# Kernel optimization log

Measured on AMD Instinct MI355X. Metric: run time of the kernel, lower is better.

## Reference

```python
import jax, jax.numpy as jnp
import numpy as np

C = 512  # channels

def _maxpool2x2(x):
    # x: [B,H,W,C] -> [B,H/2,W/2,C]
    B, H, W, Cc = x.shape
    return x.reshape(B, H // 2, 2, W // 2, 2, Cc).max(axis=(2, 4))

def setup_inputs() -> dict:
    key = jax.random.key(0)
    ks = jax.random.split(key, 6)
    x = jax.random.normal(ks[0], (16, 64, 64, C), dtype=jnp.float32)
    # 1x1 conv kernels stored as [C_in, C_out]; spectral norm treated as identity
    # on the (already-normalized) effective weights.
    s = lambda k, i, o: jax.random.normal(k, (i, o), dtype=jnp.float32) / np.sqrt(i)
    W_theta = s(ks[1], C, C // 8)
    W_phi = s(ks[2], C, C // 8)
    W_g = s(ks[3], C, C // 2)
    W_o = s(ks[4], C // 2, C)
    gamma = jnp.float32(0.7)  # nonzero so the attention path matters
    return {"x": x, "W_theta": W_theta, "W_phi": W_phi, "W_g": W_g,
            "W_o": W_o, "gamma": gamma}

def reference(x, W_theta, W_phi, W_g, W_o, gamma):
    B, H, W, Cc = x.shape
    S = H * W            # query length
    Sk = S // 4          # key/value length after 2x2 maxpool
    theta = jnp.einsum('bhwc,cd->bhwd', x, W_theta)              # [B,H,W,C/8]
    phi = _maxpool2x2(jnp.einsum('bhwc,cd->bhwd', x, W_phi))     # [B,H/2,W/2,C/8]
    g = _maxpool2x2(jnp.einsum('bhwc,cd->bhwd', x, W_g))         # [B,H/2,W/2,C/2]
    theta = theta.reshape(B, S, Cc // 8)
    phi = phi.reshape(B, Sk, Cc // 8)
    g = g.reshape(B, Sk, Cc // 2)
    # scores [B,S,Sk]; SAGAN omits the 1/sqrt(d_k) scaling
    beta = jax.nn.softmax(jnp.einsum('bqd,bkd->bqk', theta, phi), axis=-1)
    tmp = jnp.einsum('bqk,bkv->bqv', beta, g).reshape(B, H, W, Cc // 2)
    o = jnp.einsum('bhwv,vc->bhwc', tmp, W_o)
    return gamma * o + x
```

## Files before the change

kernel.cpp:

```cpp
#include <hip/hip_runtime.h>

typedef __attribute__((ext_vector_type(8))) short bf16x8;
typedef __attribute__((ext_vector_type(4))) float f32x4;
typedef unsigned short u16;
typedef unsigned int u32;

#define MFMA __builtin_amdgcn_mfma_f32_16x16x32_bf16

static __device__ __forceinline__ float b2f(u16 u) {
    u32 x = ((u32)u) << 16;
    return __builtin_bit_cast(float, x);
}
static __device__ __forceinline__ u16 f2b(float f) {
    u32 u = __builtin_bit_cast(u32, f);
    u32 r = (u + 0x7fffu + ((u >> 16) & 1u)) >> 16;
    return (u16)r;
}
static __device__ __forceinline__ void async16(const u16* g, u16* l) {
    __builtin_amdgcn_global_load_lds(
        (const __attribute__((address_space(1))) u32*)g,
        (__attribute__((address_space(3))) u32*)l, 16, 0, 0);
}

__global__ void pack_w(const float* __restrict__ Wt, const float* __restrict__ Wp,
                       const float* __restrict__ Wg, const float* __restrict__ Wo,
                       u16* __restrict__ WcatT, u16* __restrict__ WoT) {
    int t = blockIdx.x * 256 + threadIdx.x;
    const int n1 = 384 * 512;
    if (t < n1) {
        int n = t >> 9, k = t & 511;
        float v;
        if (n < 64)       v = Wt[k * 64 + n];
        else if (n < 128) v = Wp[k * 64 + (n - 64)];
        else              v = Wg[k * 256 + (n - 128)];
        WcatT[t] = f2b(v);
    } else {
        int j = t - n1;
        if (j < 512 * 256) {
            int n = j >> 8, k = j & 255;
            WoT[j] = f2b(Wo[k * 512 + n]);
        }
    }
}

template <int K>
static __device__ __forceinline__ void gemm_core(const u16* __restrict__ A,
                                                 const u16* __restrict__ Bt,
                                                 int m0, int n0, int lda, int ldb,
                                                 f32x4 acc[4][4], u16* S) {
    const int t = threadIdx.x;
    const int w = t >> 6, li = t & 15, quad = (t >> 4) & 3;
    const int wm = (w & 1) << 6, wn = (w >> 1) << 6;
#pragma unroll
    for (int mi = 0; mi < 4; mi++)
#pragma unroll
        for (int ni = 0; ni < 4; ni++) acc[mi][ni] = (f32x4)0.0f;
    const u16* ag = A + (size_t)(m0 + (t >> 2)) * lda + ((t & 3) << 3);
    const u16* bg = Bt + (size_t)(n0 + (t >> 2)) * ldb + ((t & 3) << 3);
    const int ws = w * 512;
    async16(ag, S + ws);
    async16(ag + (size_t)64 * lda, S + ws + 2048);
    async16(bg, S + 4096 + ws);
    async16(bg + (size_t)64 * ldb, S + 4096 + ws + 2048);
    __syncthreads();
    int cur = 0;
#pragma unroll
    for (int k0 = 0; k0 < K; k0 += 32) {
        if (k0 + 32 < K) {
            u16* nS = S + (cur ^ 1) * 8192;
            async16(ag + k0 + 32, nS + ws);
            async16(ag + k0 + 32 + (size_t)64 * lda, nS + ws + 2048);
            async16(bg + k0 + 32, nS + 4096 + ws);
            async16(bg + k0 + 32 + (size_t)64 * ldb, nS + 4096 + ws + 2048);
        }
        const u16* As = S + cur * 8192;
        const u16* Bs = As + 4096;
        bf16x8 af[4], bfr[4];
#pragma unroll
        for (int mi = 0; mi < 4; mi++)
            af[mi] = *(const bf16x8*)(As + (wm + mi * 16 + li) * 32 + quad * 8);
#pragma unroll
        for (int ni = 0; ni < 4; ni++)
            bfr[ni] = *(const bf16x8*)(Bs + (wn + ni * 16 + li) * 32 + quad * 8);
#pragma unroll
        for (int mi = 0; mi < 4; mi++)
#pragma unroll
            for (int ni = 0; ni < 4; ni++)
                acc[mi][ni] = MFMA(af[mi], bfr[ni], acc[mi][ni], 0, 0, 0);
        __syncthreads();
        cur ^= 1;
    }
}

template <int K>
static __device__ __forceinline__ void gemm_core_f32(const float* __restrict__ A,
                                                     const u16* __restrict__ Bt,
                                                     int m0, int n0, int lda, int ldb,
                                                     f32x4 acc[4][4], u16* S) {
    const int t = threadIdx.x;
    const int w = t >> 6, li = t & 15, quad = (t >> 4) & 3;
    const int wm = (w & 1) << 6, wn = (w >> 1) << 6;
#pragma unroll
    for (int mi = 0; mi < 4; mi++)
#pragma unroll
        for (int ni = 0; ni < 4; ni++) acc[mi][ni] = (f32x4)0.0f;
    const float* ag = A + (size_t)(m0 + (t >> 2)) * lda + ((t & 3) << 3);
    const u16* bg = Bt + (size_t)(n0 + (t >> 2)) * ldb + ((t & 3) << 3);
    const int ws = w * 512;
    {
        f32x4 a00 = *(const f32x4*)(ag);
        f32x4 a01 = *(const f32x4*)(ag + 4);
        f32x4 a10 = *(const f32x4*)(ag + (size_t)64 * lda);
        f32x4 a11 = *(const f32x4*)(ag + (size_t)64 * lda + 4);
        async16(bg, S + 4096 + ws);
        async16(bg + (size_t)64 * ldb, S + 4096 + ws + 2048);
        bf16x8 v0, v1;
#pragma unroll
        for (int e = 0; e < 4; e++) {
            v0[e] = (short)f2b(a00[e]); v0[4 + e] = (short)f2b(a01[e]);
            v1[e] = (short)f2b(a10[e]); v1[4 + e] = (short)f2b(a11[e]);
        }
        *(bf16x8*)(S + t * 8) = v0;
        *(bf16x8*)(S + 2048 + t * 8) = v1;
    }
    __syncthreads();
    int cur = 0;
#pragma unroll
    for (int k0 = 0; k0 < K; k0 += 32) {
        f32x4 a00, a01, a10, a11;
        if (k0 + 32 < K) {
            a00 = *(const f32x4*)(ag + k0 + 32);
            a01 = *(const f32x4*)(ag + k0 + 36);
            a10 = *(const f32x4*)(ag + k0 + 32 + (size_t)64 * lda);
            a11 = *(const f32x4*)(ag + k0 + 36 + (size_t)64 * lda);
            u16* nS = S + (cur ^ 1) * 8192;
            async16(bg + k0 + 32, nS + 4096 + ws);
            async16(bg + k0 + 32 + (size_t)64 * ldb, nS + 4096 + ws + 2048);
        }
        const u16* As = S + cur * 8192;
        const u16* Bs = As + 4096;
        bf16x8 af[4], bfr[4];
#pragma unroll
        for (int mi = 0; mi < 4; mi++)
            af[mi] = *(const bf16x8*)(As + (wm + mi * 16 + li) * 32 + quad * 8);
#pragma unroll
        for (int ni = 0; ni < 4; ni++)
            bfr[ni] = *(const bf16x8*)(Bs + (wn + ni * 16 + li) * 32 + quad * 8);
#pragma unroll
        for (int mi = 0; mi < 4; mi++)
#pragma unroll
            for (int ni = 0; ni < 4; ni++)
                acc[mi][ni] = MFMA(af[mi], bfr[ni], acc[mi][ni], 0, 0, 0);
        if (k0 + 32 < K) {
            u16* nS = S + (cur ^ 1) * 8192;
            bf16x8 v0, v1;
#pragma unroll
            for (int e = 0; e < 4; e++) {
                v0[e] = (short)f2b(a00[e]); v0[4 + e] = (short)f2b(a01[e]);
                v1[e] = (short)f2b(a10[e]); v1[4 + e] = (short)f2b(a11[e]);
            }
            *(bf16x8*)(nS + t * 8) = v0;
            *(bf16x8*)(nS + 2048 + t * 8) = v1;
        }
        __syncthreads();
        cur ^= 1;
    }
}

__global__ __launch_bounds__(256) void proj_gemm(const float* __restrict__ x,
                                                 const u16* __restrict__ WcatT,
                                                 u16* __restrict__ theta,
                                                 u16* __restrict__ phi,
                                                 u16* __restrict__ gT) {
    __shared__ __attribute__((aligned(16))) u16 S[16384];
    int bid = blockIdx.x;
    int sbid = (bid & 7) * 192 + (bid >> 3);
    int bm = sbid / 3, bn = sbid % 3;
    int m0 = bm * 128;
    f32x4 acc[4][4];
    gemm_core_f32<512>(x, WcatT, m0, bn * 128, 512, 512, acc, S);

    const int t = threadIdx.x;
    const int w = t >> 6, li = t & 15, quad = (t >> 4) & 3;
    const int cbase = (w >> 1) << 6;
    const int rbase = (w & 1) << 6;
#pragma unroll
    for (int mi = 0; mi < 4; mi++)
#pragma unroll
        for (int ni = 0; ni < 4; ni++) {
            int c = cbase + ni * 16 + li;
            int ch = c >> 3, ce = c & 7;
#pragma unroll
            for (int r = 0; r < 4; r++) {
                int lr = rbase + mi * 16 + quad * 4 + r;
                S[lr * 128 + ((ch ^ (lr & 7)) << 3) + ce] = f2b(acc[mi][ni][r]);
            }
        }
    __syncthreads();

    const int b = bm >> 5;
    if (bn == 0) {
        int lr = t >> 1;
#pragma unroll
        for (int k = 0; k < 4; k++) {
            int ch = (t & 1) * 4 + k;
            bf16x8 v = *(const bf16x8*)(S + lr * 128 + ((ch ^ (lr & 7)) << 3));
            *(bf16x8*)(theta + (size_t)(m0 + lr) * 64 + (t & 1) * 32 + k * 8) = v;
        }
        int w2 = t >> 3;
        int chp = 8 + (t & 7);
        int r0 = 2 * w2, r1 = r0 + 1, r2 = r0 + 64, r3 = r0 + 65;
        bf16x8 v0 = *(const bf16x8*)(S + r0 * 128 + ((chp ^ (r0 & 7)) << 3));
        bf16x8 v1 = *(const bf16x8*)(S + r1 * 128 + ((chp ^ (r1 & 7)) << 3));
        bf16x8 v2 = *(const bf16x8*)(S + r2 * 128 + ((chp ^ (r2 & 7)) << 3));
        bf16x8 v3 = *(const bf16x8*)(S + r3 * 128 + ((chp ^ (r3 & 7)) << 3));
        bf16x8 pv;
#pragma unroll
        for (int e = 0; e < 8; e++) {
            float mv = fmaxf(fmaxf(b2f((u16)v0[e]), b2f((u16)v1[e])),
                             fmaxf(b2f((u16)v2[e]), b2f((u16)v3[e])));
            pv[e] = (short)f2b(mv);
        }
        int pos2 = (bm & 31) * 32 + w2;
        *(bf16x8*)(phi + ((size_t)(b << 10) + pos2) * 64 + (t & 7) * 8) = pv;
    } else {
        const int c = t >> 1;
        const int poff = (t & 1) * 16;
        const int ch = c >> 3, ce = c & 7;
        u16 vals[16] __attribute__((aligned(16)));
#pragma unroll
        for (int j = 0; j < 16; j++) {
            int w2 = poff + j;
            int r0 = 2 * w2, r1 = r0 + 1, r2 = r0 + 64, r3 = r0 + 65;
            float m0v = b2f(S[r0 * 128 + ((ch ^ (r0 & 7)) << 3) + ce]);
            float m1v = b2f(S[r1 * 128 + ((ch ^ (r1 & 7)) << 3) + ce]);
            float m2v = b2f(S[r2 * 128 + ((ch ^ (r2 & 7)) << 3) + ce]);
            float m3v = b2f(S[r3 * 128 + ((ch ^ (r3 & 7)) << 3) + ce]);
            vals[j] = f2b(fmaxf(fmaxf(m0v, m1v), fmaxf(m2v, m3v)));
        }
        int cg = (bn - 1) * 128 + c;
        int pos2b = (bm & 31) * 32 + poff;
        u16* dst = gT + ((size_t)(b << 8) + cg) * 1024 + pos2b;
        *(uint4*)dst = *(const uint4*)vals;
        *(uint4*)(dst + 8) = *(const uint4*)(vals + 8);
    }
}

__global__ __launch_bounds__(256, 2) void attn_fused(const u16* __restrict__ theta,
                                                     const u16* __restrict__ phi,
                                                     const u16* __restrict__ gT,
                                                     u16* __restrict__ tmp) {
    __shared__ __attribute__((aligned(16))) u16 lds[28672];
    u16* stgP = lds;
    u16* stgG = lds + 4096;
    u16* pbuf = lds + 20480;

    int bid = blockIdx.x;
    int swz = (bid & 7) * 64 + (bid >> 3);
    int b = swz >> 5;
    int q0 = (swz & 31) << 7;
    const int t = threadIdx.x;
    const int w = t >> 6, li = t & 15, quad = (t >> 4) & 3;

    const u16* thp = theta + (((size_t)(b << 12) + q0 + w * 32 + li) << 6) + quad * 8;
    bf16x8 tq[2][2];
    tq[0][0] = *(const bf16x8*)thp;
    tq[0][1] = *(const bf16x8*)(thp + 32);
    tq[1][0] = *(const bf16x8*)(thp + (16 << 6));
    tq[1][1] = *(const bf16x8*)(thp + (16 << 6) + 32);

    const int srow = t >> 3;
    const int sc = (t & 7) ^ (srow & 7);
    const u16* phisrc = phi + ((size_t)(b << 10) + srow) * 64 + sc * 8;
    const u16* gsrc = gT + ((size_t)(b << 8) + srow) * 1024 + sc * 8;
    u16* pbq[2] = {pbuf + (w * 2 + 0) * 1024, pbuf + (w * 2 + 1) * 1024};

    f32x4 o[2][16];
#pragma unroll
    for (int qg = 0; qg < 2; qg++)
#pragma unroll
        for (int ni = 0; ni < 16; ni++) o[qg][ni] = (f32x4)0.0f;
    float m[2] = {-3.0e38f, -3.0e38f}, sum[2] = {0.0f, 0.0f};

    for (int kc = 0; kc < 16; kc++) {
        __syncthreads();
        async16(phisrc + (size_t)(kc * 64) * 64, stgP + w * 512);
        async16(phisrc + (size_t)(kc * 64 + 32) * 64, stgP + 2048 + w * 512);
#pragma unroll
        for (int j = 0; j < 8; j++)
            async16(gsrc + (size_t)(j * 32) * 1024 + kc * 64, stgG + j * 2048 + w * 512);
        __syncthreads();

        f32x4 sacc[2][4];
#pragma unroll
        for (int qg = 0; qg < 2; qg++)
#pragma unroll
            for (int nf = 0; nf < 4; nf++) sacc[qg][nf] = (f32x4)0.0f;
#pragma unroll
        for (int nf = 0; nf < 4; nf++) {
            int row = nf * 16 + li;
            int p0 = quad ^ (li & 7);
            int p1 = (4 + quad) ^ (li & 7);
            bf16x8 f0 = *(const bf16x8*)(stgP + row * 64 + p0 * 8);
            bf16x8 f1 = *(const bf16x8*)(stgP + row * 64 + p1 * 8);
            sacc[0][nf] = MFMA(f0, tq[0][0], sacc[0][nf], 0, 0, 0);
            sacc[0][nf] = MFMA(f1, tq[0][1], sacc[0][nf], 0, 0, 0);
            sacc[1][nf] = MFMA(f0, tq[1][0], sacc[1][nf], 0, 0, 0);
            sacc[1][nf] = MFMA(f1, tq[1][1], sacc[1][nf], 0, 0, 0);
        }

#pragma unroll
        for (int qg = 0; qg < 2; qg++) {
            float mc = sacc[qg][0][0];
#pragma unroll
            for (int nf = 0; nf < 4; nf++)
#pragma unroll
                for (int r = 0; r < 4; r++) mc = fmaxf(mc, sacc[qg][nf][r]);
            mc = fmaxf(mc, __shfl_xor(mc, 16, 64));
            mc = fmaxf(mc, __shfl_xor(mc, 32, 64));
            if (!__all(mc <= m[qg] + 8.0f)) {
                float nm = fmaxf(m[qg], mc);
                float f = __expf(m[qg] - nm);
                sum[qg] *= f;
#pragma unroll
                for (int ni = 0; ni < 16; ni++)
#pragma unroll
                    for (int r = 0; r < 4; r++) o[qg][ni][r] *= f;
                m[qg] = nm;
            }
            float p[16];
            float s = 0.0f;
#pragma unroll
            for (int nf = 0; nf < 4; nf++)
#pragma unroll
                for (int r = 0; r < 4; r++) {
                    float e = __expf(sacc[qg][nf][r] - m[qg]);
                    p[nf * 4 + r] = e;
                    s += e;
                }
            s += __shfl_xor(s, 16, 64);
            s += __shfl_xor(s, 32, 64);
            sum[qg] += s;

            u16* pb = pbq[qg];
#pragma unroll
            for (int nf = 0; nf < 4; nf++) {
                int cc = nf * 2 + (quad >> 1);
                int pos = cc ^ (li & 7);
                u32* dst = (u32*)(pb + li * 64 + pos * 8 + (quad & 1) * 4);
                dst[0] = (u32)f2b(p[nf * 4 + 0]) | ((u32)f2b(p[nf * 4 + 1]) << 16);
                dst[1] = (u32)f2b(p[nf * 4 + 2]) | ((u32)f2b(p[nf * 4 + 3]) << 16);
            }
        }

#pragma unroll
        for (int w2 = 0; w2 < 2; w2++) {
            int pos8 = ((w2 * 4 + quad) ^ (li & 7)) * 8;
            bf16x8 pf0 = *(const bf16x8*)(pbq[0] + li * 64 + pos8);
            bf16x8 pf1 = *(const bf16x8*)(pbq[1] + li * 64 + pos8);
#pragma unroll
            for (int ni = 0; ni < 16; ni++) {
                bf16x8 gf = *(const bf16x8*)(stgG + (ni * 16 + li) * 64 + pos8);
                o[0][ni] = MFMA(gf, pf0, o[0][ni], 0, 0, 0);
                o[1][ni] = MFMA(gf, pf1, o[1][ni], 0, 0, 0);
            }
        }
    }

    float inv[2] = {1.0f / sum[0], 1.0f / sum[1]};
#pragma unroll
    for (int qg = 0; qg < 2; qg++)
#pragma unroll
        for (int ni = 0; ni < 16; ni++)
#pragma unroll
            for (int r = 0; r < 4; r++) o[qg][ni][r] *= inv[qg];

    __syncthreads();
    u16* eb = lds + w * 4224;
    const int lane = t & 63;
#pragma unroll
    for (int qg = 0; qg < 2; qg++) {
#pragma unroll
        for (int ni = 0; ni < 16; ni++) {
            u32* d = (u32*)(eb + li * 264 + ni * 16 + quad * 4);
            d[0] = (u32)f2b(o[qg][ni][0]) | ((u32)f2b(o[qg][ni][1]) << 16);
            d[1] = (u32)f2b(o[qg][ni][2]) | ((u32)f2b(o[qg][ni][3]) << 16);
        }
#pragma unroll
        for (int pss = 0; pss < 8; pss++) {
            int row = pss * 2 + (lane >> 5);
            bf16x8 v = *(const bf16x8*)(eb + row * 264 + (lane & 31) * 8);
            *(bf16x8*)(tmp + ((size_t)(b << 12) + q0 + w * 32 + qg * 16 + row) * 256 +
                       (lane & 31) * 8) = v;
        }
    }
}

__global__ __launch_bounds__(256) void out_gemm(const u16* __restrict__ tmp,
                                                const u16* __restrict__ WoT,
                                                const float* __restrict__ x,
                                                const float* __restrict__ gamma_p,
                                                float* __restrict__ out) {
    __shared__ __attribute__((aligned(16))) u16 sbuf[16384];
    int bid = blockIdx.x;
    int sbid = (bid & 7) * 256 + (bid >> 3);
    int bm = sbid >> 2, bn = sbid & 3;
    f32x4 acc[4][4];
    gemm_core<256>(tmp, WoT, bm * 128, bn * 128, 256, 256, acc, sbuf);
    float gamma = gamma_p[0];
    const int t = threadIdx.x;
    const int w = t >> 6, li = t & 15, quad = (t >> 4) & 3;
    int row0 = bm * 128 + (w & 1) * 64;
    int col0 = bn * 128 + (w >> 1) * 64;
    float* fb = (float*)sbuf + w * 1088;
    const int lane = t & 63;
    const int rhi = lane >> 4, cl = (lane & 15) * 4;
#pragma unroll
    for (int mi = 0; mi < 4; mi++) {
        f32x4 xv[4];
#pragma unroll
        for (int j = 0; j < 4; j++) {
            size_t go = (size_t)(row0 + mi * 16 + j * 4 + rhi) * 512 + col0 + cl;
            xv[j] = *(const f32x4*)(x + go);
        }
#pragma unroll
        for (int ni = 0; ni < 4; ni++)
#pragma unroll
            for (int r = 0; r < 4; r++)
                fb[(quad * 4 + r) * 68 + ni * 16 + li] = acc[mi][ni][r];
#pragma unroll
        for (int j = 0; j < 4; j++) {
            f32x4 v = *(const f32x4*)(fb + (j * 4 + rhi) * 68 + cl);
#pragma unroll
            for (int e = 0; e < 4; e++) v[e] = gamma * v[e] + xv[j][e];
            size_t go = (size_t)(row0 + mi * 16 + j * 4 + rhi) * 512 + col0 + cl;
            *(f32x4*)(out + go) = v;
        }
    }
}

extern "C" void kernel_launch(void* const* d_in, const int* in_sizes, int n_in,
                              void* d_out, int out_size, void* d_ws, size_t ws_size,
                              hipStream_t stream) {
    (void)in_sizes; (void)n_in; (void)out_size; (void)ws_size;
    const float* x  = (const float*)d_in[0];
    const float* Wt = (const float*)d_in[1];
    const float* Wp = (const float*)d_in[2];
    const float* Wg = (const float*)d_in[3];
    const float* Wo = (const float*)d_in[4];
    const float* gm = (const float*)d_in[5];
    float* out = (float*)d_out;

    char* ws = (char*)d_ws;
    size_t off = 0;
    u16* WcatT = (u16*)(ws + off); off += (size_t)384 * 512 * 2;
    u16* WoT   = (u16*)(ws + off); off += (size_t)512 * 256 * 2;
    u16* phi   = (u16*)(ws + off); off += (size_t)16 * 1024 * 64 * 2;
    u16* gT    = (u16*)(ws + off); off += (size_t)16 * 256 * 1024 * 2;
    u16* theta = (u16*)(ws + off); off += (size_t)65536 * 64 * 2;
    u16* tmp   = (u16*)(ws + off); off += (size_t)65536 * 256 * 2;

    pack_w<<<1280, 256, 0, stream>>>(Wt, Wp, Wg, Wo, WcatT, WoT);
    proj_gemm<<<1536, 256, 0, stream>>>(x, WcatT, theta, phi, gT);
    attn_fused<<<512, 256, 0, stream>>>(theta, phi, gT, tmp);
    out_gemm<<<2048, 256, 0, stream>>>(tmp, WoT, x, gm, out);
}
```

Measured before the change: 356.6 us.

## Load phi and g fragments directly from global, drop shared staging and barriers

The attention kernel no longer stages the phi and gT tiles in shared memory with async loads and two block-wide barriers per key chunk. Each wave now reads its MFMA operand fragments straight from global memory (relying on L1/L2 caching across the four waves), and s_setprio brackets are placed around the MFMA sections. This removes the synchronisation and the LDS traffic, at the cost of each wave separately fetching the same phi/g data from cache, with uncoalesced 16-byte loads and exposed global latency. Shared memory shrinks to the P buffers plus the epilogue area.

```diff
diff --git a/kernel.cpp b/kernel.cpp
--- a/kernel.cpp
+++ b/kernel.cpp
@@ -250,11 +250,7 @@
                                                      const u16* __restrict__ phi,
                                                      const u16* __restrict__ gT,
                                                      u16* __restrict__ tmp) {
-    __shared__ __attribute__((aligned(16))) u16 lds[28672];
-    u16* stgP = lds;
-    u16* stgG = lds + 4096;
-    u16* pbuf = lds + 20480;
-
+    __shared__ __attribute__((aligned(16))) u16 lds[25088];
     int bid = blockIdx.x;
     int swz = (bid & 7) * 64 + (bid >> 3);
     int b = swz >> 5;
@@ -269,11 +265,9 @@
     tq[1][0] = *(const bf16x8*)(thp + (16 << 6));
     tq[1][1] = *(const bf16x8*)(thp + (16 << 6) + 32);
 
-    const int srow = t >> 3;
-    const int sc = (t & 7) ^ (srow & 7);
-    const u16* phisrc = phi + ((size_t)(b << 10) + srow) * 64 + sc * 8;
-    const u16* gsrc = gT + ((size_t)(b << 8) + srow) * 1024 + sc * 8;
-    u16* pbq[2] = {pbuf + (w * 2 + 0) * 1024, pbuf + (w * 2 + 1) * 1024};
+    const u16* pRow = phi + ((size_t)(b << 10) + li) * 64 + quad * 8;
+    const u16* gRow = gT + ((size_t)(b << 8) + li) * 1024;
+    u16* pbq[2] = {lds + (w * 2 + 0) * 1024, lds + (w * 2 + 1) * 1024};
 
     f32x4 o[2][16];
 #pragma unroll
@@ -283,31 +277,23 @@
     float m[2] = {-3.0e38f, -3.0e38f}, sum[2] = {0.0f, 0.0f};
 
     for (int kc = 0; kc < 16; kc++) {
-        __syncthreads();
-        async16(phisrc + (size_t)(kc * 64) * 64, stgP + w * 512);
-        async16(phisrc + (size_t)(kc * 64 + 32) * 64, stgP + 2048 + w * 512);
-#pragma unroll
-        for (int j = 0; j < 8; j++)
-            async16(gsrc + (size_t)(j * 32) * 1024 + kc * 64, stgG + j * 2048 + w * 512);
-        __syncthreads();
-
         f32x4 sacc[2][4];
 #pragma unroll
         for (int qg = 0; qg < 2; qg++)
 #pragma unroll
             for (int nf = 0; nf < 4; nf++) sacc[qg][nf] = (f32x4)0.0f;
+        __builtin_amdgcn_s_setprio(1);
 #pragma unroll
         for (int nf = 0; nf < 4; nf++) {
-            int row = nf * 16 + li;
-            int p0 = quad ^ (li & 7);
-            int p1 = (4 + quad) ^ (li & 7);
-            bf16x8 f0 = *(const bf16x8*)(stgP + row * 64 + p0 * 8);
-            bf16x8 f1 = *(const bf16x8*)(stgP + row * 64 + p1 * 8);
+            const u16* pr = pRow + (size_t)(kc * 64 + nf * 16) * 64;
+            bf16x8 f0 = *(const bf16x8*)pr;
+            bf16x8 f1 = *(const bf16x8*)(pr + 32);
             sacc[0][nf] = MFMA(f0, tq[0][0], sacc[0][nf], 0, 0, 0);
             sacc[0][nf] = MFMA(f1, tq[0][1], sacc[0][nf], 0, 0, 0);
             sacc[1][nf] = MFMA(f0, tq[1][0], sacc[1][nf], 0, 0, 0);
             sacc[1][nf] = MFMA(f1, tq[1][1], sacc[1][nf], 0, 0, 0);
         }
+        __builtin_amdgcn_s_setprio(0);
 
 #pragma unroll
         for (int qg = 0; qg < 2; qg++) {
@@ -353,18 +339,21 @@
             }
         }
 
+        __builtin_amdgcn_s_setprio(1);
 #pragma unroll
         for (int w2 = 0; w2 < 2; w2++) {
             int pos8 = ((w2 * 4 + quad) ^ (li & 7)) * 8;
             bf16x8 pf0 = *(const bf16x8*)(pbq[0] + li * 64 + pos8);
             bf16x8 pf1 = *(const bf16x8*)(pbq[1] + li * 64 + pos8);
+            const u16* gp = gRow + kc * 64 + (w2 * 4 + quad) * 8;
 #pragma unroll
             for (int ni = 0; ni < 16; ni++) {
-                bf16x8 gf = *(const bf16x8*)(stgG + (ni * 16 + li) * 64 + pos8);
+                bf16x8 gf = *(const bf16x8*)(gp + (size_t)(ni * 16) * 1024);
                 o[0][ni] = MFMA(gf, pf0, o[0][ni], 0, 0, 0);
                 o[1][ni] = MFMA(gf, pf1, o[1][ni], 0, 0, 0);
             }
         }
+        __builtin_amdgcn_s_setprio(0);
     }
 
     float inv[2] = {1.0f / sum[0], 1.0f / sum[1]};
@@ -375,8 +364,7 @@
 #pragma unroll
             for (int r = 0; r < 4; r++) o[qg][ni][r] *= inv[qg];
 
-    __syncthreads();
-    u16* eb = lds + w * 4224;
+    u16* eb = lds + 8192 + w * 4224;
     const int lane = t & 63;
 #pragma unroll
     for (int qg = 0; qg < 2; qg++) {
```

Measured after the change: 449.6 us. 1.26x slower.
